# Kernel tuning notes

Measured on AMD Instinct MI355X. Metric: run time of the kernel, lower is better.

## Reference

```python
import jax, jax.numpy as jnp
import numpy as np

N_NODES = 100000
N_EDGES = 640000
F_IN = 128
HID = 128
N_CLS = 40


def _glorot(key, fan_in, fan_out):
    lim = float(np.sqrt(6.0 / (fan_in + fan_out)))
    return jax.random.uniform(key, (fan_in, fan_out), jnp.float32, -lim, lim)


def setup_inputs() -> dict:
    key = jax.random.key(0)
    ks = jax.random.split(key, 10)
    x = jax.random.normal(ks[0], (N_NODES, F_IN), jnp.float32)
    edge_index = jax.random.randint(ks[1], (2, N_EDGES), 0, N_NODES, jnp.int64 if jax.config.jax_enable_x64 else jnp.int32)
    W1 = _glorot(ks[2], F_IN, HID)
    W2 = _glorot(ks[3], HID, HID)
    W3 = _glorot(ks[4], HID, HID)
    W4 = _glorot(ks[5], HID, N_CLS)
    b1 = jnp.zeros((HID,), jnp.float32)
    b2 = jnp.zeros((HID,), jnp.float32)
    b3 = jnp.zeros((HID,), jnp.float32)
    b4 = jnp.zeros((N_CLS,), jnp.float32)
    return {"x": x, "edge_index": edge_index,
            "W1": W1, "b1": b1, "W2": W2, "b2": b2,
            "W3": W3, "b3": b3, "W4": W4, "b4": b4}


def _prep_edges(edge_index, n):
    # add self-loops, compute symmetric normalization deg^{-1/2}[src]*deg^{-1/2}[dst]
    loop = jnp.arange(n, dtype=edge_index.dtype)
    src = jnp.concatenate([edge_index[0], loop])
    dst = jnp.concatenate([edge_index[1], loop])
    deg = jax.ops.segment_sum(jnp.ones_like(dst, jnp.float32), dst, num_segments=n)
    dinv = jnp.where(deg > 0, jax.lax.rsqrt(deg), 0.0)
    norm = dinv[src] * dinv[dst]  # [E + n]
    return src, dst, norm


def _gcn_conv(x, W, b, src, dst, norm, n):
    h = x @ W                      # dense linear transform [n, out]
    msg = h[src] * norm[:, None]   # gather + scale over edges
    out = jax.ops.segment_sum(msg, dst, num_segments=n)  # scatter-add
    return out + b


def reference(x, edge_index, W1, b1, W2, b2, W3, b3, W4, b4):
    n = x.shape[0]
    src, dst, norm = _prep_edges(edge_index, n)
    h = jax.nn.relu(_gcn_conv(x, W1, b1, src, dst, norm, n))
    h = jax.nn.relu(_gcn_conv(h, W2, b2, src, dst, norm, n))
    h = jax.nn.relu(_gcn_conv(h, W3, b3, src, dst, norm, n))
    h = _gcn_conv(h, W4, b4, src, dst, norm, n)
    return jax.nn.log_softmax(h, axis=1)
```

## Files before the change

### kernel.cpp

```cpp
#include <hip/hip_runtime.h>
#include <math.h>

#define N_NODES 100000
#define N_EDGES 640000

typedef __bf16 bf16x8 __attribute__((ext_vector_type(8)));
typedef float f32x4 __attribute__((ext_vector_type(4)));

__device__ __forceinline__ unsigned short f2b(float x) {
  unsigned int u = __float_as_uint(x);
  u = (u + 0x7FFFu + ((u >> 16) & 1u)) >> 16;
  return (unsigned short)u;
}
__device__ __forceinline__ float blo(unsigned int v) { return __uint_as_float(v << 16); }
__device__ __forceinline__ float bhi(unsigned int v) { return __uint_as_float(v & 0xFFFF0000u); }

__device__ __forceinline__ int fragidx(int nn, int k) {
  int ct = nn >> 4, m = nn & 15;
  int kc = k >> 5, q = (k >> 3) & 3, e = k & 7;
  return (((ct * 4 + kc) * 4 + q) * 16 + m) * 8 + e;
}


__global__ __launch_bounds__(256) void k_count(const int* __restrict__ dst, int* __restrict__ deg, int e) {
  int i = blockIdx.x * 256 + threadIdx.x;
  if (i < e) atomicAdd(&deg[dst[i]], 1);
}

__global__ __launch_bounds__(256) void k_alloc(const int* __restrict__ deg, int* __restrict__ row_ptr,
                                               int* __restrict__ fillpos, int* __restrict__ col,
                                               float* __restrict__ dinv, int* __restrict__ counter, int n) {
  __shared__ int sdata[256];
  __shared__ int sbase;
  int tid = threadIdx.x;
  int i = blockIdx.x * 256 + tid;
  int d = (i < n) ? deg[i] : 0;
  sdata[tid] = d;
  __syncthreads();
  for (int off = 1; off < 256; off <<= 1) {
    int v = (tid >= off) ? sdata[tid - off] : 0;
    __syncthreads();
    sdata[tid] += v;
    __syncthreads();
  }
  if (tid == 255) sbase = atomicAdd(counter, sdata[255]);
  __syncthreads();
  int base = sbase;
  if (i < n) {
    int rp = base + sdata[tid] - d;
    row_ptr[i] = rp;
    fillpos[i] = rp + 1;
    col[rp] = i;
    dinv[i] = rsqrtf((float)d);
  }
}

__global__ __launch_bounds__(256) void k_fill(const int* __restrict__ src, const int* __restrict__ dst,
                                              int* __restrict__ fillpos, int* __restrict__ col, int e) {
  int i = blockIdx.x * 256 + threadIdx.x;
  if (i < e) {
    int d = dst[i];
    int p = atomicAdd(&fillpos[d], 1);
    col[p] = src[i];
  }
}


__global__ __launch_bounds__(256) void k_prep0(const float* __restrict__ W1, const float* __restrict__ W2,
                                               const float* __restrict__ W3, const float* __restrict__ W4,
                                               unsigned short* __restrict__ Wt, unsigned short* __restrict__ Wt4,
                                               unsigned short* __restrict__ Ha, unsigned short* __restrict__ Hc,
                                               unsigned short* __restrict__ H4,
                                               int* __restrict__ deg, int* __restrict__ counter, int n) {
  int b = blockIdx.x;
  int tid = threadIdx.x;
  if (b < 391) {
    int i = b * 256 + tid;
    if (i < n) deg[i] = 1;
    if (i == 0) *counter = 0;
  } else if (b < 583) {
    int bb = b - 391;
    const float* W = (bb < 64) ? W1 : (bb < 128) ? W2 : W3;
    unsigned short* D = Wt + ((bb < 64) ? 0 : (bb < 128) ? 16384 : 32768);
    int idx = (bb & 63) * 256 + tid;
    int k = idx >> 7, nn = idx & 127;
    D[fragidx(nn, k)] = f2b(W[idx]);
  } else if (b < 607) {
    int idx = (b - 583) * 256 + tid;
    int nn = idx >> 7, k = idx & 127;
    Wt4[fragidx(nn, k)] = (nn < 40) ? f2b(W4[(size_t)k * 40 + nn]) : (unsigned short)0;
  } else if (b == 607) {
    if (tid < 128) Ha[(size_t)n * 128 + tid] = 0;
    else Hc[(size_t)n * 128 + (tid - 128)] = 0;
  } else {
    if (tid < 48) H4[(size_t)n * 40 + tid] = 0;
  }
}

#define SXP 136


__global__ __launch_bounds__(256) void k_gemm1(const float* __restrict__ X,
                                               const unsigned short* __restrict__ Wt,
                                               const float* __restrict__ dinv,
                                               unsigned short* __restrict__ H, int n) {
  int tid = threadIdx.x;
  int row0 = blockIdx.x * 64;
  int wave = tid >> 6, lane = tid & 63;
  int m = lane & 15, q = lane >> 4;
  int grow = row0 + wave * 16 + m;
  if (grow >= n) grow = n - 1;
  const float4* X4 = (const float4*)X;
  uint4 a4[4];
#pragma unroll
  for (int kc = 0; kc < 4; ++kc) {
    float4 f0 = X4[(size_t)grow * 32 + kc * 8 + q * 2];
    float4 f1 = X4[(size_t)grow * 32 + kc * 8 + q * 2 + 1];
    a4[kc].x = (unsigned int)f2b(f0.x) | ((unsigned int)f2b(f0.y) << 16);
    a4[kc].y = (unsigned int)f2b(f0.z) | ((unsigned int)f2b(f0.w) << 16);
    a4[kc].z = (unsigned int)f2b(f1.x) | ((unsigned int)f2b(f1.y) << 16);
    a4[kc].w = (unsigned int)f2b(f1.z) | ((unsigned int)f2b(f1.w) << 16);
  }
  const bf16x8* Wf = (const bf16x8*)Wt;
  f32x4 acc[8];
#pragma unroll
  for (int ct = 0; ct < 8; ++ct) acc[ct] = (f32x4){0.f, 0.f, 0.f, 0.f};
#pragma unroll
  for (int kc = 0; kc < 4; ++kc) {
    bf16x8 a = *(bf16x8*)&a4[kc];
#pragma unroll
    for (int ct = 0; ct < 8; ++ct) {
      bf16x8 b = Wf[(ct * 4 + kc) * 64 + lane];
      acc[ct] = __builtin_amdgcn_mfma_f32_16x16x32_bf16(a, b, acc[ct], 0, 0, 0);
    }
  }
#pragma unroll
  for (int r = 0; r < 4; ++r) {
    int row = row0 + wave * 16 + q * 4 + r;
    if (row < n) {
      float di = dinv[row];
#pragma unroll
      for (int ct = 0; ct < 8; ++ct)
        H[(size_t)row * 128 + ct * 16 + m] = f2b(acc[ct][r] * di);
    }
  }
}


template <int NCT>
__global__ __launch_bounds__(256) void k_fag(const unsigned short* __restrict__ Hin,
                                             const int* __restrict__ col,
                                             const int* __restrict__ row_ptr,
                                             const int* __restrict__ deg,
                                             const float* __restrict__ dinv,
                                             const float* __restrict__ bias,
                                             const unsigned short* __restrict__ Wt,
                                             unsigned short* __restrict__ Hout, int n) {
  __shared__ unsigned short sX[64 * SXP];
  int tid = threadIdx.x;
  int row0 = blockIdx.x * 64;
  int ql = tid & 15;
  int qbase = tid & 48;
  const uint4* Hg = (const uint4*)Hin;
  float4 b0 = ((const float4*)bias)[ql * 2];
  float4 b1 = ((const float4*)bias)[ql * 2 + 1];
  int starts[4], cnts[4], mycs[4];
#pragma unroll
  for (int it = 0; it < 4; ++it) {
    int node = row0 + (tid >> 4) + (it << 4);
    int nc = (node < n) ? node : 0;
    starts[it] = row_ptr[nc];
    cnts[it] = deg[nc];
  }
#pragma unroll
  for (int it = 0; it < 4; ++it) {
    int c0 = (cnts[it] < 15) ? cnts[it] : 15;
    mycs[it] = (ql < c0) ? col[starts[it] + ql] : n;
  }
#pragma unroll 1
  for (int it = 0; it < 4; ++it) {
    int node = row0 + (tid >> 4) + (it << 4);
    if (node >= n) break;
    int cnt = cnts[it];
    int cnt0 = (cnt < 15) ? cnt : 15;
    int myc = mycs[it];
    float s0 = 0.f, s1 = 0.f, s2 = 0.f, s3 = 0.f, s4 = 0.f, s5 = 0.f, s6 = 0.f, s7 = 0.f;
    for (int base = 0; base < cnt0; base += 8) {
      uint4 v[8];
#pragma unroll
      for (int jj = 0; jj < 8; ++jj) {
        int idx = base + jj;
        idx = (idx > 15) ? 15 : idx;
        int c = __shfl(myc, qbase + idx, 64);
        v[jj] = Hg[(size_t)c * 16 + ql];
      }
#pragma unroll
      for (int jj = 0; jj < 8; ++jj) {
        s0 += blo(v[jj].x); s1 += bhi(v[jj].x);
        s2 += blo(v[jj].y); s3 += bhi(v[jj].y);
        s4 += blo(v[jj].z); s5 += bhi(v[jj].z);
        s6 += blo(v[jj].w); s7 += bhi(v[jj].w);
      }
    }
    for (int j = 15; j < cnt; ++j) {
      int c = col[starts[it] + j];
      uint4 v = Hg[(size_t)c * 16 + ql];
      s0 += blo(v.x); s1 += bhi(v.x);
      s2 += blo(v.y); s3 += bhi(v.y);
      s4 += blo(v.z); s5 += bhi(v.z);
      s6 += blo(v.w); s7 += bhi(v.w);
    }
    float di = dinv[node];
    float o0 = fmaf(s0, di, b0.x), o1 = fmaf(s1, di, b0.y);
    float o2 = fmaf(s2, di, b0.z), o3 = fmaf(s3, di, b0.w);
    float o4 = fmaf(s4, di, b1.x), o5 = fmaf(s5, di, b1.y);
    float o6 = fmaf(s6, di, b1.z), o7 = fmaf(s7, di, b1.w);
    o0 = o0 > 0.f ? o0 : 0.f; o1 = o1 > 0.f ? o1 : 0.f;
    o2 = o2 > 0.f ? o2 : 0.f; o3 = o3 > 0.f ? o3 : 0.f;
    o4 = o4 > 0.f ? o4 : 0.f; o5 = o5 > 0.f ? o5 : 0.f;
    o6 = o6 > 0.f ? o6 : 0.f; o7 = o7 > 0.f ? o7 : 0.f;
    uint4 w;
    w.x = (unsigned int)f2b(o0) | ((unsigned int)f2b(o1) << 16);
    w.y = (unsigned int)f2b(o2) | ((unsigned int)f2b(o3) << 16);
    w.z = (unsigned int)f2b(o4) | ((unsigned int)f2b(o5) << 16);
    w.w = (unsigned int)f2b(o6) | ((unsigned int)f2b(o7) << 16);
    *(uint4*)&sX[(node - row0) * SXP + ql * 8] = w;
  }
  __syncthreads();
  int wave = tid >> 6, lane = tid & 63;
  int m = lane & 15, q = lane >> 4;
  int grow = row0 + wave * 16 + m;
  if (grow >= n) grow = n - 1;
  int lrow = grow - row0;
  uint4 a4[4];
#pragma unroll
  for (int kc = 0; kc < 4; ++kc) a4[kc] = *(const uint4*)&sX[lrow * SXP + kc * 32 + q * 8];
  const bf16x8* Wf = (const bf16x8*)Wt;
  f32x4 acc[NCT];
#pragma unroll
  for (int ct = 0; ct < NCT; ++ct) acc[ct] = (f32x4){0.f, 0.f, 0.f, 0.f};
#pragma unroll
  for (int kc = 0; kc < 4; ++kc) {
    bf16x8 a = *(bf16x8*)&a4[kc];
#pragma unroll
    for (int ct = 0; ct < NCT; ++ct) {
      bf16x8 b = Wf[(ct * 4 + kc) * 64 + lane];
      acc[ct] = __builtin_amdgcn_mfma_f32_16x16x32_bf16(a, b, acc[ct], 0, 0, 0);
    }
  }
#pragma unroll
  for (int r = 0; r < 4; ++r) {
    int row = row0 + wave * 16 + q * 4 + r;
    if (row < n) {
      float di = dinv[row];
      if constexpr (NCT == 8) {
#pragma unroll
        for (int ct = 0; ct < 8; ++ct)
          Hout[(size_t)row * 128 + ct * 16 + m] = f2b(acc[ct][r] * di);
      } else {
#pragma unroll
        for (int ct = 0; ct < NCT; ++ct) {
          int c = ct * 16 + m;
          if (c < 40) Hout[(size_t)row * 40 + c] = f2b(acc[ct][r] * di);
        }
      }
    }
  }
}


__global__ __launch_bounds__(256) void k_agg40_lsm(const unsigned short* __restrict__ H, const int* __restrict__ col,
                                                   const int* __restrict__ row_ptr, const int* __restrict__ deg,
                                                   const float* __restrict__ dinv, const float* __restrict__ bias,
                                                   float* __restrict__ out, int n) {
  int node = blockIdx.x * 4 + (threadIdx.x >> 6);
  int lane = threadIdx.x & 63;
  if (node >= n) return;
  const unsigned int* H1 = (const unsigned int*)H;
  int start = row_ptr[node];
  int cnt = deg[node];
  int cnt0 = (cnt < 63) ? cnt : 63;
  int myc = (lane < cnt0) ? col[start + lane] : n;
  int slice = (lane >= 20) + (lane >= 40);
  int pr = lane - slice * 20;
  pr = (pr > 19) ? 19 : pr;
  int rounds = (cnt0 + 2) / 3;
  float ax = 0.f, ay = 0.f;
  for (int rb = 0; rb < rounds; rb += 4) {
    unsigned int v[4];
#pragma unroll
    for (int j = 0; j < 4; ++j) {
      int idx = (rb + j) * 3 + slice;
      idx = (idx > 63) ? 63 : idx;
      int c = __shfl(myc, idx, 64);
      v[j] = H1[(size_t)c * 20 + pr];
    }
#pragma unroll
    for (int j = 0; j < 4; ++j) { ax += blo(v[j]); ay += bhi(v[j]); }
  }
  if (lane < 20) {
    for (int j = 63; j < cnt; ++j) {
      int c = col[start + j];
      unsigned int v = H1[(size_t)c * 20 + pr];
      ax += blo(v);
      ay += bhi(v);
    }
  }
  float ax1 = __shfl(ax, lane + 20, 64), ay1 = __shfl(ay, lane + 20, 64);
  float ax2 = __shfl(ax, lane + 40, 64), ay2 = __shfl(ay, lane + 40, 64);
  float di = dinv[node];
  float2 b2 = ((const float2*)bias)[pr];
  float c0 = fmaf(ax + ax1 + ax2, di, b2.x);
  float c1 = fmaf(ay + ay1 + ay2, di, b2.y);
  float v = (lane < 20) ? fmaxf(c0, c1) : -INFINITY;
#pragma unroll
  for (int off = 32; off > 0; off >>= 1) v = fmaxf(v, __shfl_xor(v, off, 64));
  float e = (lane < 20) ? (__expf(c0 - v) + __expf(c1 - v)) : 0.f;
#pragma unroll
  for (int off = 32; off > 0; off >>= 1) e += __shfl_xor(e, off, 64);
  if (lane < 20) {
    float ls = v + __logf(e);
    ((float2*)out)[(size_t)node * 20 + lane] = make_float2(c0 - ls, c1 - ls);
  }
}


extern "C" void kernel_launch(void* const* d_in, const int* in_sizes, int n_in,
                              void* d_out, int out_size, void* d_ws, size_t ws_size,
                              hipStream_t stream) {
  const float* x  = (const float*)d_in[0];
  const int* edge = (const int*)d_in[1];
  const float* W1 = (const float*)d_in[2];
  const float* b1 = (const float*)d_in[3];
  const float* W2 = (const float*)d_in[4];
  const float* b2 = (const float*)d_in[5];
  const float* W3 = (const float*)d_in[6];
  const float* b3 = (const float*)d_in[7];
  const float* W4 = (const float*)d_in[8];
  const float* b4 = (const float*)d_in[9];
  float* out = (float*)d_out;

  const int n = N_NODES, E = N_EDGES;
  const int* srcp = edge;
  const int* dstp = edge + E;

  char* ws = (char*)d_ws;
  size_t off = 0;
  auto alloc = [&](size_t bytes) -> void* {
    void* p = ws + off;
    off = (off + bytes + 255) & ~(size_t)255;
    return p;
  };
  int*   deg     = (int*)alloc((size_t)n * 4);
  int*   row_ptr = (int*)alloc((size_t)n * 4);
  int*   fillpos = (int*)alloc((size_t)n * 4);
  float* dinv    = (float*)alloc((size_t)n * 4);
  int*   counter = (int*)alloc(256);
  int*   colx    = (int*)alloc((size_t)(E + n) * 4);
  unsigned short* Ha  = (unsigned short*)alloc((size_t)(n + 1) * 128 * 2);
  unsigned short* Hc  = (unsigned short*)alloc((size_t)(n + 1) * 128 * 2);
  unsigned short* H4  = (unsigned short*)alloc(((size_t)(n + 1) * 40 + 16) * 2);
  unsigned short* Wt  = (unsigned short*)alloc((size_t)3 * 128 * 128 * 2);
  unsigned short* Wt4 = (unsigned short*)alloc((size_t)48 * 128 * 2);
  (void)ws_size; (void)in_sizes; (void)n_in; (void)out_size;

  k_prep0<<<609, 256, 0, stream>>>(W1, W2, W3, W4, Wt, Wt4, Ha, Hc, H4, deg, counter, n);
  k_count<<<(E + 255) / 256, 256, 0, stream>>>(dstp, deg, E);
  k_alloc<<<(n + 255) / 256, 256, 0, stream>>>(deg, row_ptr, fillpos, colx, dinv, counter, n);
  k_fill <<<(E + 255) / 256, 256, 0, stream>>>(srcp, dstp, fillpos, colx, E);

  const int gg = (n + 63) / 64, ga = (n + 3) / 4;
  k_gemm1<<<gg, 256, 0, stream>>>(x, Wt, dinv, Ha, n);
  k_fag<8><<<gg, 256, 0, stream>>>(Ha, colx, row_ptr, deg, dinv, b1, Wt + 16384, Hc, n);
  k_fag<8><<<gg, 256, 0, stream>>>(Hc, colx, row_ptr, deg, dinv, b2, Wt + 32768, Ha, n);
  k_fag<3><<<gg, 256, 0, stream>>>(Ha, colx, row_ptr, deg, dinv, b3, Wt4, H4, n);
  k_agg40_lsm<<<ga, 256, 0, stream>>>(H4, colx, row_ptr, deg, dinv, b4, out, n);
}
```

Before: 340.6 us.

## Batch neighbor gathers across all four rows and stage weights in LDS

The fused aggregate+GEMM kernel now issues the first eight neighbor-row gathers for all four node slots up front, keeping 32 uint4 loads in flight per thread instead of one row batch at a time. While those loads are pending, it copies the weight fragments into shared memory, and the MFMA loop then reads B operands from LDS rather than global memory. The second batch of up to seven neighbors is still loaded per row. The cost is much higher register pressure (v[4][8] uint4), which may cut occupancy, plus extra LDS use for the weights.

```diff
diff --git a/kernel.cpp b/kernel.cpp
--- a/kernel.cpp
+++ b/kernel.cpp
@@ -156,75 +156,102 @@
                                              const float* __restrict__ bias,
                                              const unsigned short* __restrict__ Wt,
                                              unsigned short* __restrict__ Hout, int n) {
+  __shared__ unsigned short sW[NCT * 2048];
   __shared__ unsigned short sX[64 * SXP];
   int tid = threadIdx.x;
   int row0 = blockIdx.x * 64;
   int ql = tid & 15;
   int qbase = tid & 48;
   const uint4* Hg = (const uint4*)Hin;
-  float4 b0 = ((const float4*)bias)[ql * 2];
-  float4 b1 = ((const float4*)bias)[ql * 2 + 1];
   int starts[4], cnts[4], mycs[4];
+  float dinvs[4];
 #pragma unroll
   for (int it = 0; it < 4; ++it) {
     int node = row0 + (tid >> 4) + (it << 4);
     int nc = (node < n) ? node : 0;
     starts[it] = row_ptr[nc];
     cnts[it] = deg[nc];
+    dinvs[it] = dinv[nc];
   }
 #pragma unroll
   for (int it = 0; it < 4; ++it) {
     int c0 = (cnts[it] < 15) ? cnts[it] : 15;
     mycs[it] = (ql < c0) ? col[starts[it] + ql] : n;
   }
-#pragma unroll 1
+  uint4 v[4][8];
+#pragma unroll
+  for (int it = 0; it < 4; ++it) {
+#pragma unroll
+    for (int jj = 0; jj < 8; ++jj) {
+      int c = __shfl(mycs[it], qbase + jj, 64);
+      v[it][jj] = Hg[(size_t)c * 16 + ql];
+    }
+  }
+  {
+    const uint4* W4 = (const uint4*)Wt;
+    uint4* sW4 = (uint4*)sW;
+#pragma unroll
+    for (int i = 0; i < NCT; ++i) sW4[i * 256 + tid] = W4[i * 256 + tid];
+  }
+  float4 b0 = ((const float4*)bias)[ql * 2];
+  float4 b1 = ((const float4*)bias)[ql * 2 + 1];
+#pragma unroll
   for (int it = 0; it < 4; ++it) {
     int node = row0 + (tid >> 4) + (it << 4);
-    if (node >= n) break;
     int cnt = cnts[it];
     int cnt0 = (cnt < 15) ? cnt : 15;
     int myc = mycs[it];
+    bool r2 = (cnt0 > 8);
+    uint4 w2[8];
+    if (r2) {
+#pragma unroll
+      for (int jj = 0; jj < 8; ++jj) {
+        int c = __shfl(myc, qbase + 8 + jj, 64);
+        w2[jj] = Hg[(size_t)c * 16 + ql];
+      }
+    }
     float s0 = 0.f, s1 = 0.f, s2 = 0.f, s3 = 0.f, s4 = 0.f, s5 = 0.f, s6 = 0.f, s7 = 0.f;
-    for (int base = 0; base < cnt0; base += 8) {
-      uint4 v[8];
+#pragma unroll
+    for (int jj = 0; jj < 8; ++jj) {
+      s0 += blo(v[it][jj].x); s1 += bhi(v[it][jj].x);
+      s2 += blo(v[it][jj].y); s3 += bhi(v[it][jj].y);
+      s4 += blo(v[it][jj].z); s5 += bhi(v[it][jj].z);
+      s6 += blo(v[it][jj].w); s7 += bhi(v[it][jj].w);
+    }
+    if (r2) {
 #pragma unroll
       for (int jj = 0; jj < 8; ++jj) {
-        int idx = base + jj;
-        idx = (idx > 15) ? 15 : idx;
-        int c = __shfl(myc, qbase + idx, 64);
-        v[jj] = Hg[(size_t)c * 16 + ql];
-      }
-#pragma unroll
-      for (int jj = 0; jj < 8; ++jj) {
-        s0 += blo(v[jj].x); s1 += bhi(v[jj].x);
-        s2 += blo(v[jj].y); s3 += bhi(v[jj].y);
-        s4 += blo(v[jj].z); s5 += bhi(v[jj].z);
-        s6 += blo(v[jj].w); s7 += bhi(v[jj].w);
+        s0 += blo(w2[jj].x); s1 += bhi(w2[jj].x);
+        s2 += blo(w2[jj].y); s3 += bhi(w2[jj].y);
+        s4 += blo(w2[jj].z); s5 += bhi(w2[jj].z);
+        s6 += blo(w2[jj].w); s7 += bhi(w2[jj].w);
       }
     }
     for (int j = 15; j < cnt; ++j) {
       int c = col[starts[it] + j];
-      uint4 v = Hg[(size_t)c * 16 + ql];
-      s0 += blo(v.x); s1 += bhi(v.x);
-      s2 += blo(v.y); s3 += bhi(v.y);
-      s4 += blo(v.z); s5 += bhi(v.z);
-      s6 += blo(v.w); s7 += bhi(v.w);
-    }
-    float di = dinv[node];
-    float o0 = fmaf(s0, di, b0.x), o1 = fmaf(s1, di, b0.y);
-    float o2 = fmaf(s2, di, b0.z), o3 = fmaf(s3, di, b0.w);
-    float o4 = fmaf(s4, di, b1.x), o5 = fmaf(s5, di, b1.y);
-    float o6 = fmaf(s6, di, b1.z), o7 = fmaf(s7, di, b1.w);
-    o0 = o0 > 0.f ? o0 : 0.f; o1 = o1 > 0.f ? o1 : 0.f;
-    o2 = o2 > 0.f ? o2 : 0.f; o3 = o3 > 0.f ? o3 : 0.f;
-    o4 = o4 > 0.f ? o4 : 0.f; o5 = o5 > 0.f ? o5 : 0.f;
-    o6 = o6 > 0.f ? o6 : 0.f; o7 = o7 > 0.f ? o7 : 0.f;
-    uint4 w;
-    w.x = (unsigned int)f2b(o0) | ((unsigned int)f2b(o1) << 16);
-    w.y = (unsigned int)f2b(o2) | ((unsigned int)f2b(o3) << 16);
-    w.z = (unsigned int)f2b(o4) | ((unsigned int)f2b(o5) << 16);
-    w.w = (unsigned int)f2b(o6) | ((unsigned int)f2b(o7) << 16);
-    *(uint4*)&sX[(node - row0) * SXP + ql * 8] = w;
+      uint4 t = Hg[(size_t)c * 16 + ql];
+      s0 += blo(t.x); s1 += bhi(t.x);
+      s2 += blo(t.y); s3 += bhi(t.y);
+      s4 += blo(t.z); s5 += bhi(t.z);
+      s6 += blo(t.w); s7 += bhi(t.w);
+    }
+    if (node < n) {
+      float di = dinvs[it];
+      float o0 = fmaf(s0, di, b0.x), o1 = fmaf(s1, di, b0.y);
+      float o2 = fmaf(s2, di, b0.z), o3 = fmaf(s3, di, b0.w);
+      float o4 = fmaf(s4, di, b1.x), o5 = fmaf(s5, di, b1.y);
+      float o6 = fmaf(s6, di, b1.z), o7 = fmaf(s7, di, b1.w);
+      o0 = o0 > 0.f ? o0 : 0.f; o1 = o1 > 0.f ? o1 : 0.f;
+      o2 = o2 > 0.f ? o2 : 0.f; o3 = o3 > 0.f ? o3 : 0.f;
+      o4 = o4 > 0.f ? o4 : 0.f; o5 = o5 > 0.f ? o5 : 0.f;
+      o6 = o6 > 0.f ? o6 : 0.f; o7 = o7 > 0.f ? o7 : 0.f;
+      uint4 w;
+      w.x = (unsigned int)f2b(o0) | ((unsigned int)f2b(o1) << 16);
+      w.y = (unsigned int)f2b(o2) | ((unsigned int)f2b(o3) << 16);
+      w.z = (unsigned int)f2b(o4) | ((unsigned int)f2b(o5) << 16);
+      w.w = (unsigned int)f2b(o6) | ((unsigned int)f2b(o7) << 16);
+      *(uint4*)&sX[(node - row0) * SXP + ql * 8] = w;
+    }
   }
   __syncthreads();
   int wave = tid >> 6, lane = tid & 63;
@@ -235,7 +262,7 @@
   uint4 a4[4];
 #pragma unroll
   for (int kc = 0; kc < 4; ++kc) a4[kc] = *(const uint4*)&sX[lrow * SXP + kc * 32 + q * 8];
-  const bf16x8* Wf = (const bf16x8*)Wt;
+  const bf16x8* Wl = (const bf16x8*)sW;
   f32x4 acc[NCT];
 #pragma unroll
   for (int ct = 0; ct < NCT; ++ct) acc[ct] = (f32x4){0.f, 0.f, 0.f, 0.f};
@@ -244,7 +271,7 @@
     bf16x8 a = *(bf16x8*)&a4[kc];
 #pragma unroll
     for (int ct = 0; ct < NCT; ++ct) {
-      bf16x8 b = Wf[(ct * 4 + kc) * 64 + lane];
+      bf16x8 b = Wl[(ct * 4 + kc) * 64 + lane];
       acc[ct] = __builtin_amdgcn_mfma_f32_16x16x32_bf16(a, b, acc[ct], 0, 0, 0);
     }
   }
```

After: 341.3 us. No clear change (+0.2%).

## Split fused aggregate-GEMM into sliced-layout aggregation and separate GEMM kernels

Applied to the files above, without the earlier changes.

Stores hidden features in a column-sliced layout (8 slices of 16 features per node) so each aggregation block gathers only 32-byte pieces of one slice, aiming for better cache locality in the random gather. The former fused aggregate+GEMM kernel becomes two kernels: a per-slice aggregation and a GEMM that stages weights in shared memory. This adds an extra intermediate buffer round-trip through global memory and three extra launches in exchange for a smaller per-pass gather working set.

```diff
diff --git a/kernel.cpp b/kernel.cpp
--- a/kernel.cpp
+++ b/kernel.cpp
@@ -20,6 +20,7 @@
   int kc = k >> 5, q = (k >> 3) & 3, e = k & 7;
   return (((ct * 4 + kc) * 4 + q) * 16 + m) * 8 + e;
 }
+
 
 
 __global__ __launch_bounds__(256) void k_count(const int* __restrict__ dst, int* __restrict__ deg, int e) {
@@ -90,8 +91,12 @@
     int nn = idx >> 7, k = idx & 127;
     Wt4[fragidx(nn, k)] = (nn < 40) ? f2b(W4[(size_t)k * 40 + nn]) : (unsigned short)0;
   } else if (b == 607) {
-    if (tid < 128) Ha[(size_t)n * 128 + tid] = 0;
-    else Hc[(size_t)n * 128 + (tid - 128)] = 0;
+    size_t RS = (size_t)(n + 1) * 16;
+    int which = tid >> 7;
+    int idx = tid & 127;
+    int s = idx >> 4, o = idx & 15;
+    unsigned short* P = which ? Hc : Ha;
+    P[(size_t)s * RS + (size_t)n * 16 + o] = 0;
   } else {
     if (tid < 48) H4[(size_t)n * 40 + tid] = 0;
   }
@@ -134,6 +139,7 @@
       acc[ct] = __builtin_amdgcn_mfma_f32_16x16x32_bf16(a, b, acc[ct], 0, 0, 0);
     }
   }
+  size_t RS = (size_t)(n + 1) * 16;
 #pragma unroll
   for (int r = 0; r < 4; ++r) {
     int row = row0 + wave * 16 + q * 4 + r;
@@ -141,101 +147,93 @@
       float di = dinv[row];
 #pragma unroll
       for (int ct = 0; ct < 8; ++ct)
-        H[(size_t)row * 128 + ct * 16 + m] = f2b(acc[ct][r] * di);
-    }
-  }
+        H[(size_t)ct * RS + (size_t)row * 16 + m] = f2b(acc[ct][r] * di);
+    }
+  }
+}
+
+
+__global__ __launch_bounds__(256) void k_aggs(const unsigned short* __restrict__ Hin,
+                                              const int* __restrict__ col,
+                                              const int* __restrict__ row_ptr,
+                                              const int* __restrict__ deg,
+                                              const float* __restrict__ dinv,
+                                              const float* __restrict__ bias,
+                                              unsigned short* __restrict__ Xout, int n) {
+  int s = blockIdx.x & 7;
+  int g = blockIdx.x >> 3;
+  int node = g * 128 + (threadIdx.x >> 1);
+  int half = threadIdx.x & 1;
+  if (node >= n) return;
+  const size_t RS = (size_t)(n + 1) * 16;
+  const size_t RSX = (size_t)n * 16;
+  const uint4* Hs = (const uint4*)(Hin + (size_t)s * RS);
+  int start = row_ptr[node];
+  int cnt = deg[node];
+  float a0 = 0.f, a1 = 0.f, a2 = 0.f, a3 = 0.f, a4 = 0.f, a5 = 0.f, a6 = 0.f, a7 = 0.f;
+  for (int j = 0; j < cnt; j += 8) {
+    uint4 v[8];
+#pragma unroll
+    for (int k2 = 0; k2 < 8; ++k2) {
+      int jj = j + k2;
+      int c = (jj < cnt) ? col[start + jj] : n;
+      v[k2] = Hs[(size_t)c * 2 + half];
+    }
+#pragma unroll
+    for (int k2 = 0; k2 < 8; ++k2) {
+      a0 += blo(v[k2].x); a1 += bhi(v[k2].x);
+      a2 += blo(v[k2].y); a3 += bhi(v[k2].y);
+      a4 += blo(v[k2].z); a5 += bhi(v[k2].z);
+      a6 += blo(v[k2].w); a7 += bhi(v[k2].w);
+    }
+  }
+  float di = dinv[node];
+  const float4* B4 = (const float4*)(bias + s * 16 + half * 8);
+  float4 bb0 = B4[0], bb1 = B4[1];
+  float o0 = fmaf(a0, di, bb0.x), o1 = fmaf(a1, di, bb0.y);
+  float o2 = fmaf(a2, di, bb0.z), o3 = fmaf(a3, di, bb0.w);
+  float o4 = fmaf(a4, di, bb1.x), o5 = fmaf(a5, di, bb1.y);
+  float o6 = fmaf(a6, di, bb1.z), o7 = fmaf(a7, di, bb1.w);
+  o0 = o0 > 0.f ? o0 : 0.f; o1 = o1 > 0.f ? o1 : 0.f;
+  o2 = o2 > 0.f ? o2 : 0.f; o3 = o3 > 0.f ? o3 : 0.f;
+  o4 = o4 > 0.f ? o4 : 0.f; o5 = o5 > 0.f ? o5 : 0.f;
+  o6 = o6 > 0.f ? o6 : 0.f; o7 = o7 > 0.f ? o7 : 0.f;
+  uint4 w;
+  w.x = (unsigned int)f2b(o0) | ((unsigned int)f2b(o1) << 16);
+  w.y = (unsigned int)f2b(o2) | ((unsigned int)f2b(o3) << 16);
+  w.z = (unsigned int)f2b(o4) | ((unsigned int)f2b(o5) << 16);
+  w.w = (unsigned int)f2b(o6) | ((unsigned int)f2b(o7) << 16);
+  *(uint4*)&Xout[(size_t)s * RSX + (size_t)node * 16 + half * 8] = w;
 }
 
 
 template <int NCT>
-__global__ __launch_bounds__(256) void k_fag(const unsigned short* __restrict__ Hin,
-                                             const int* __restrict__ col,
-                                             const int* __restrict__ row_ptr,
-                                             const int* __restrict__ deg,
-                                             const float* __restrict__ dinv,
-                                             const float* __restrict__ bias,
-                                             const unsigned short* __restrict__ Wt,
-                                             unsigned short* __restrict__ Hout, int n) {
-  __shared__ unsigned short sX[64 * SXP];
+__global__ __launch_bounds__(256) void k_gemms(const unsigned short* __restrict__ X,
+                                               const unsigned short* __restrict__ Wt,
+                                               const float* __restrict__ dinv,
+                                               unsigned short* __restrict__ Hout, int n) {
+  __shared__ unsigned short sW[NCT * 2048];
   int tid = threadIdx.x;
   int row0 = blockIdx.x * 64;
-  int ql = tid & 15;
-  int qbase = tid & 48;
-  const uint4* Hg = (const uint4*)Hin;
-  float4 b0 = ((const float4*)bias)[ql * 2];
-  float4 b1 = ((const float4*)bias)[ql * 2 + 1];
-  int starts[4], cnts[4], mycs[4];
-#pragma unroll
-  for (int it = 0; it < 4; ++it) {
-    int node = row0 + (tid >> 4) + (it << 4);
-    int nc = (node < n) ? node : 0;
-    starts[it] = row_ptr[nc];
-    cnts[it] = deg[nc];
-  }
-#pragma unroll
-  for (int it = 0; it < 4; ++it) {
-    int c0 = (cnts[it] < 15) ? cnts[it] : 15;
-    mycs[it] = (ql < c0) ? col[starts[it] + ql] : n;
-  }
-#pragma unroll 1
-  for (int it = 0; it < 4; ++it) {
-    int node = row0 + (tid >> 4) + (it << 4);
-    if (node >= n) break;
-    int cnt = cnts[it];
-    int cnt0 = (cnt < 15) ? cnt : 15;
-    int myc = mycs[it];
-    float s0 = 0.f, s1 = 0.f, s2 = 0.f, s3 = 0.f, s4 = 0.f, s5 = 0.f, s6 = 0.f, s7 = 0.f;
-    for (int base = 0; base < cnt0; base += 8) {
-      uint4 v[8];
-#pragma unroll
-      for (int jj = 0; jj < 8; ++jj) {
-        int idx = base + jj;
-        idx = (idx > 15) ? 15 : idx;
-        int c = __shfl(myc, qbase + idx, 64);
-        v[jj] = Hg[(size_t)c * 16 + ql];
-      }
-#pragma unroll
-      for (int jj = 0; jj < 8; ++jj) {
-        s0 += blo(v[jj].x); s1 += bhi(v[jj].x);
-        s2 += blo(v[jj].y); s3 += bhi(v[jj].y);
-        s4 += blo(v[jj].z); s5 += bhi(v[jj].z);
-        s6 += blo(v[jj].w); s7 += bhi(v[jj].w);
-      }
-    }
-    for (int j = 15; j < cnt; ++j) {
-      int c = col[starts[it] + j];
-      uint4 v = Hg[(size_t)c * 16 + ql];
-      s0 += blo(v.x); s1 += bhi(v.x);
-      s2 += blo(v.y); s3 += bhi(v.y);
-      s4 += blo(v.z); s5 += bhi(v.z);
-      s6 += blo(v.w); s7 += bhi(v.w);
-    }
-    float di = dinv[node];
-    float o0 = fmaf(s0, di, b0.x), o1 = fmaf(s1, di, b0.y);
-    float o2 = fmaf(s2, di, b0.z), o3 = fmaf(s3, di, b0.w);
-    float o4 = fmaf(s4, di, b1.x), o5 = fmaf(s5, di, b1.y);
-    float o6 = fmaf(s6, di, b1.z), o7 = fmaf(s7, di, b1.w);
-    o0 = o0 > 0.f ? o0 : 0.f; o1 = o1 > 0.f ? o1 : 0.f;
-    o2 = o2 > 0.f ? o2 : 0.f; o3 = o3 > 0.f ? o3 : 0.f;
-    o4 = o4 > 0.f ? o4 : 0.f; o5 = o5 > 0.f ? o5 : 0.f;
-    o6 = o6 > 0.f ? o6 : 0.f; o7 = o7 > 0.f ? o7 : 0.f;
-    uint4 w;
-    w.x = (unsigned int)f2b(o0) | ((unsigned int)f2b(o1) << 16);
-    w.y = (unsigned int)f2b(o2) | ((unsigned int)f2b(o3) << 16);
-    w.z = (unsigned int)f2b(o4) | ((unsigned int)f2b(o5) << 16);
-    w.w = (unsigned int)f2b(o6) | ((unsigned int)f2b(o7) << 16);
-    *(uint4*)&sX[(node - row0) * SXP + ql * 8] = w;
-  }
-  __syncthreads();
+  {
+    const uint4* W4 = (const uint4*)Wt;
+    uint4* sW4 = (uint4*)sW;
+#pragma unroll
+    for (int i = 0; i < NCT; ++i) sW4[i * 256 + tid] = W4[i * 256 + tid];
+  }
   int wave = tid >> 6, lane = tid & 63;
   int m = lane & 15, q = lane >> 4;
   int grow = row0 + wave * 16 + m;
   if (grow >= n) grow = n - 1;
-  int lrow = grow - row0;
+  const size_t RSX = (size_t)n * 16;
   uint4 a4[4];
 #pragma unroll
-  for (int kc = 0; kc < 4; ++kc) a4[kc] = *(const uint4*)&sX[lrow * SXP + kc * 32 + q * 8];
-  const bf16x8* Wf = (const bf16x8*)Wt;
+  for (int kc = 0; kc < 4; ++kc) {
+    int s = kc * 2 + (q >> 1);
+    a4[kc] = *(const uint4*)&X[(size_t)s * RSX + (size_t)grow * 16 + (q & 1) * 8];
+  }
+  __syncthreads();
+  const bf16x8* Wl = (const bf16x8*)sW;
   f32x4 acc[NCT];
 #pragma unroll
   for (int ct = 0; ct < NCT; ++ct) acc[ct] = (f32x4){0.f, 0.f, 0.f, 0.f};
@@ -244,7 +242,7 @@
     bf16x8 a = *(bf16x8*)&a4[kc];
 #pragma unroll
     for (int ct = 0; ct < NCT; ++ct) {
-      bf16x8 b = Wf[(ct * 4 + kc) * 64 + lane];
+      bf16x8 b = Wl[(ct * 4 + kc) * 64 + lane];
       acc[ct] = __builtin_amdgcn_mfma_f32_16x16x32_bf16(a, b, acc[ct], 0, 0, 0);
     }
   }
@@ -254,9 +252,10 @@
     if (row < n) {
       float di = dinv[row];
       if constexpr (NCT == 8) {
+        size_t RS = (size_t)(n + 1) * 16;
 #pragma unroll
         for (int ct = 0; ct < 8; ++ct)
-          Hout[(size_t)row * 128 + ct * 16 + m] = f2b(acc[ct][r] * di);
+          Hout[(size_t)ct * RS + (size_t)row * 16 + m] = f2b(acc[ct][r] * di);
       } else {
 #pragma unroll
         for (int ct = 0; ct < NCT; ++ct) {
@@ -359,6 +358,7 @@
   int*   colx    = (int*)alloc((size_t)(E + n) * 4);
   unsigned short* Ha  = (unsigned short*)alloc((size_t)(n + 1) * 128 * 2);
   unsigned short* Hc  = (unsigned short*)alloc((size_t)(n + 1) * 128 * 2);
+  unsigned short* Xc  = (unsigned short*)alloc((size_t)n * 128 * 2);
   unsigned short* H4  = (unsigned short*)alloc(((size_t)(n + 1) * 40 + 16) * 2);
   unsigned short* Wt  = (unsigned short*)alloc((size_t)3 * 128 * 128 * 2);
   unsigned short* Wt4 = (unsigned short*)alloc((size_t)48 * 128 * 2);
@@ -369,10 +369,15 @@
   k_alloc<<<(n + 255) / 256, 256, 0, stream>>>(deg, row_ptr, fillpos, colx, dinv, counter, n);
   k_fill <<<(E + 255) / 256, 256, 0, stream>>>(srcp, dstp, fillpos, colx, E);
 
-  const int gg = (n + 63) / 64, ga = (n + 3) / 4;
+  const int gg = (n + 63) / 64;
+  const int gs = 8 * ((n + 127) / 128);
+  const int ga = (n + 3) / 4;
   k_gemm1<<<gg, 256, 0, stream>>>(x, Wt, dinv, Ha, n);
-  k_fag<8><<<gg, 256, 0, stream>>>(Ha, colx, row_ptr, deg, dinv, b1, Wt + 16384, Hc, n);
-  k_fag<8><<<gg, 256, 0, stream>>>(Hc, colx, row_ptr, deg, dinv, b2, Wt + 32768, Ha, n);
-  k_fag<3><<<gg, 256, 0, stream>>>(Ha, colx, row_ptr, deg, dinv, b3, Wt4, H4, n);
+  k_aggs <<<gs, 256, 0, stream>>>(Ha, colx, row_ptr, deg, dinv, b1, Xc, n);
+  k_gemms<8><<<gg, 256, 0, stream>>>(Xc, Wt + 16384, dinv, Hc, n);
+  k_aggs <<<gs, 256, 0, stream>>>(Hc, colx, row_ptr, deg, dinv, b2, Xc, n);
+  k_gemms<8><<<gg, 256, 0, stream>>>(Xc, Wt + 32768, dinv, Ha, n);
+  k_aggs <<<gs, 256, 0, stream>>>(Ha, colx, row_ptr, deg, dinv, b3, Xc, n);
+  k_gemms<3><<<gg, 256, 0, stream>>>(Xc, Wt4, dinv, H4, n);
   k_agg40_lsm<<<ga, 256, 0, stream>>>(H4, colx, row_ptr, deg, dinv, b4, out, n);
 }
```

Result: slower. 388.0 us (+13.9%).
